# Kernel tuning notes

Measured on AMD Instinct MI355X. Metric: run time of the kernel, lower is better.

Reference implementation:

```python
import jax, jax.numpy as jnp
import numpy as np

FOCAL = 1015.0
IMG = 256


def setup_inputs() -> dict:
    key = jax.random.key(0)
    ks = jax.random.split(key, 9)
    B, NV, NF = 128, 35709, 70789
    coeff = jax.random.normal(ks[0], (B, 257), jnp.float32) * 0.1
    meanshape = jax.random.normal(ks[1], (NV * 3,), jnp.float32)
    idBase = jax.random.normal(ks[2], (NV * 3, 80), jnp.float32) * 0.01
    exBase = jax.random.normal(ks[3], (NV * 3, 64), jnp.float32) * 0.01
    meantex = jax.random.uniform(ks[4], (NV * 3,), jnp.float32) * 255.0
    texBase = jax.random.normal(ks[5], (NV * 3, 80), jnp.float32)
    # 1-based indices, matching the facemodel convention (code subtracts 1)
    tri = jax.random.randint(ks[6], (NF, 3), 1, NV + 1, jnp.int32)
    # point_buf may reference the appended zero face (index NF+1, 1-based)
    point_buf = jax.random.randint(ks[7], (NV, 8), 1, NF + 2, jnp.int32)
    kp_inds = jax.random.randint(ks[8], (68,), 0, NV, jnp.int32)
    return dict(coeff=coeff, meanshape=meanshape, idBase=idBase, exBase=exBase,
                meantex=meantex, texBase=texBase, tri=tri, point_buf=point_buf,
                kp_inds=kp_inds)


def _rotation(angles):
    # rotation = (Rz @ Ry @ Rx)^T, per Compute_rotation_matrix
    sx, sy, sz = jnp.sin(angles[:, 0]), jnp.sin(angles[:, 1]), jnp.sin(angles[:, 2])
    cx, cy, cz = jnp.cos(angles[:, 0]), jnp.cos(angles[:, 1]), jnp.cos(angles[:, 2])
    o, l = jnp.zeros_like(sx), jnp.ones_like(sx)
    Rx = jnp.stack([l, o, o, o, cx, -sx, o, sx, cx], -1).reshape(-1, 3, 3)
    Ry = jnp.stack([cy, o, sy, o, l, o, -sy, o, cy], -1).reshape(-1, 3, 3)
    Rz = jnp.stack([cz, -sz, o, sz, cz, o, o, o, l], -1).reshape(-1, 3, 3)
    return jnp.einsum('bij,bjk,bkl->bli', Rz, Ry, Rx)


def _compute_norm(shape, tri, point_buf):
    fid = tri - 1  # [F,3] 0-based vertex ids
    v1 = shape[:, fid[:, 0]]  # [B,F,3]
    v2 = shape[:, fid[:, 1]]
    v3 = shape[:, fid[:, 2]]
    fn = jnp.cross(v1 - v2, v2 - v3)  # per-face normals [B,F,3]
    fn = jnp.concatenate([fn, jnp.zeros_like(fn[:, :1])], axis=1)  # pad zero face
    vn = fn[:, point_buf - 1].sum(axis=2)  # [B,NV,8,3] -> [B,NV,3]
    return vn / jnp.linalg.norm(vn, axis=2, keepdims=True)


def _illumination(tex, norm, gamma):
    B, N, _ = tex.shape
    gamma = gamma.reshape(B, 3, 9).at[:, :, 0].add(0.8).transpose(0, 2, 1)  # [B,9,3]
    a0 = np.pi
    a1 = 2.0 * np.pi / np.sqrt(3.0)
    a2 = 2.0 * np.pi / np.sqrt(8.0)
    c0 = 1.0 / np.sqrt(4.0 * np.pi)
    c1 = np.sqrt(3.0) / np.sqrt(4.0 * np.pi)
    c2 = 3.0 * np.sqrt(5.0) / np.sqrt(12.0 * np.pi)
    d0 = 0.5 / np.sqrt(3.0)
    nx, ny, nz = norm[..., 0], norm[..., 1], norm[..., 2]
    Y = jnp.stack([
        jnp.full_like(nx, np.float32(a0 * c0)),
        -a1 * c1 * ny,
        a1 * c1 * nz,
        -a1 * c1 * nx,
        a2 * c2 * nx * ny,
        -a2 * c2 * ny * nz,
        a2 * c2 * d0 * (3.0 * nz ** 2 - 1.0),
        -a2 * c2 * nx * nz,
        a2 * c2 * 0.5 * (nx ** 2 - ny ** 2),
    ], axis=-1)  # [B,N,9]
    lighting = jnp.einsum('bnc,bcd->bnd', Y, gamma)  # [B,N,3]
    return tex * lighting


def _project(pts):
    half = IMG // 2
    pts = pts * jnp.array([1.0, 1.0, -1.0], jnp.float32) + jnp.array([0.0, 0.0, 10.0], jnp.float32)
    P = jnp.array([[FOCAL, 0.0, half], [0.0, FOCAL, half], [0.0, 0.0, 1.0]], jnp.float32)
    aug = pts @ P.T
    return aug[..., :2] / aug[..., 2:3]


def reference(coeff, meanshape, idBase, exBase, meantex, texBase, tri, point_buf, kp_inds):
    B = coeff.shape[0]
    idc, exc, texc = coeff[:, :80], coeff[:, 80:144], coeff[:, 144:224]
    angles, gamma, trans = coeff[:, 224:227], coeff[:, 227:254], coeff[:, 254:257]
    # Shape_formation
    shape = (idc @ idBase.T + exc @ exBase.T + meanshape).reshape(B, -1, 3)
    shape = shape - meanshape.reshape(1, -1, 3).mean(axis=1, keepdims=True)
    # Texture_formation
    tex = (texc @ texBase.T + meantex).reshape(B, -1, 3)
    # Normals, rotation, rigid transform
    vnorm = _compute_norm(shape, tri, point_buf)
    rot = _rotation(angles)  # [B,3,3]
    vnorm_r = jnp.einsum('bnc,bcd->bnd', vnorm, rot)
    shape_t = jnp.einsum('bnc,bcd->bnd', shape, rot) + trans[:, None, :]
    # Illumination (vertex colors) and landmark projection
    face_color = _illumination(tex, vnorm_r, gamma)
    lms = _project(shape_t[:, kp_inds])
    lms = jnp.stack([lms[..., 0], IMG - lms[..., 1]], axis=-1)
    return face_color, lms, shape_t
```

## Files before the change

### kernel.cpp

```cpp
#include <hip/hip_runtime.h>

typedef unsigned short u16;
typedef unsigned int u32;
typedef __attribute__((ext_vector_type(8))) short bfrag;
typedef __attribute__((ext_vector_type(4))) float ffrag;
typedef __attribute__((ext_vector_type(4))) float f4;
typedef __attribute__((ext_vector_type(2))) float f2;
typedef __attribute__((ext_vector_type(2))) u32 u32x2;
typedef __attribute__((ext_vector_type(4))) int i4;

#define NVERT 35709
#define NFACE 70789
#define NV3   107127
#define NB    128

#define SHAPE_OFF 0ull
#define TEX4_OFF  54849024ull
#define FXY_OFF   91415040ull
#define FZ_OFF    127659008ull
#define CPACK_OFF 145780992ull
#define MPAD_OFF  145846528ull
#define GG_OFF    145852672ull
#define MEAN_OFF  145866496ull
#define PART_OFF  145866512ull

#define LMS_BASE  13712256ull
#define ST_BASE   13729664ull

__device__ __forceinline__ float b2f(u16 s) {
  union { unsigned u; float f; } v; v.u = ((unsigned)s) << 16; return v.f;
}
__device__ __forceinline__ u16 f2b(float x) {
  union { float f; unsigned u; } v; v.f = x;
  unsigned r = v.u + 0x7FFFu + ((v.u >> 16) & 1u);
  return (u16)(r >> 16);
}
__device__ __forceinline__ u16 h2b(float x) {
  union { _Float16 h; u16 u; } v; v.h = (_Float16)x; return v.u;
}
__device__ __forceinline__ float hb2f(u16 u) {
  union { _Float16 h; u16 u2; } v; v.u2 = u; return (float)v.h;
}
__device__ __forceinline__ f4 ld4u(const float* p) {
  f4 r; __builtin_memcpy(&r, p, 16); return r;
}
__device__ __forceinline__ bfrag cvt8c(const float* p) {
  f4 a = *(const f4*)p;
  f4 b = *(const f4*)(p + 4);
  bfrag r;
  r[0] = (short)f2b(a.x); r[1] = (short)f2b(a.y); r[2] = (short)f2b(a.z); r[3] = (short)f2b(a.w);
  r[4] = (short)f2b(b.x); r[5] = (short)f2b(b.y); r[6] = (short)f2b(b.z); r[7] = (short)f2b(b.w);
  return r;
}

__global__ __launch_bounds__(256) void k_mean(const float* __restrict__ ms, float* __restrict__ part) {
  __shared__ float s[3];
  if (threadIdx.x < 3) s[threadIdx.x] = 0.f;
  __syncthreads();
  float a0 = 0.f, a1 = 0.f, a2 = 0.f;
  for (int v = blockIdx.x * 256 + threadIdx.x; v < NVERT; v += 64 * 256) {
    a0 += ms[v * 3 + 0];
    a1 += ms[v * 3 + 1];
    a2 += ms[v * 3 + 2];
  }
  atomicAdd(&s[0], a0); atomicAdd(&s[1], a1); atomicAdd(&s[2], a2);
  __syncthreads();
  if (threadIdx.x < 3) part[blockIdx.x * 3 + threadIdx.x] = s[threadIdx.x];
}

__global__ __launch_bounds__(128) void k_params(const float* __restrict__ coeff, u16* __restrict__ cpack,
                                                float* __restrict__ mpad, float* __restrict__ G,
                                                const float* __restrict__ part, float* __restrict__ mean) {
  int b = threadIdx.x;
  if (b < 3) {
    float s = 0.f;
    for (int i = 0; i < 64; i++) s += part[i * 3 + b];
    mean[b] = s * (1.0f / (float)NVERT);
  }
  const float* c = coeff + b * 257;
  u16* cp = cpack + b * 256;
  for (int k = 0; k < 80; k++) cp[k] = f2b(c[k]);
  for (int k = 80; k < 96; k++) cp[k] = 0;
  for (int k = 0; k < 64; k++) cp[96 + k] = f2b(c[80 + k]);
  for (int k = 0; k < 80; k++) cp[160 + k] = f2b(c[144 + k]);
  for (int k = 240; k < 256; k++) cp[k] = 0;
  float ax = c[224], ay = c[225], az = c[226];
  float sx = sinf(ax), cx = cosf(ax);
  float sy = sinf(ay), cy = cosf(ay);
  float sz = sinf(az), cz = cosf(az);
  float* mp = mpad + b * 12;
  mp[0] = cz * cy;  mp[1] = cz * sy * sx - sz * cx;  mp[2] = sz * sx + cz * sy * cx;
  mp[3] = sz * cy;  mp[4] = cz * cx + sz * sy * sx;  mp[5] = sz * sy * cx - cz * sx;
  mp[6] = -sy;      mp[7] = cy * sx;                 mp[8] = cy * cx;
  mp[9] = c[254]; mp[10] = c[255]; mp[11] = c[256];
  float* g = G + b * 27;
  for (int cc = 0; cc < 9; cc++)
    for (int d = 0; d < 3; d++)
      g[cc * 3 + d] = c[227 + d * 9 + cc] + (cc == 0 ? 0.8f : 0.0f);
}

#define SBLK 558
__global__ __launch_bounds__(256) void k_gemmS(const float* __restrict__ idB, const float* __restrict__ exB,
                                               const float* __restrict__ ms, const u16* __restrict__ cpack,
                                               const float* __restrict__ meanc, const float* __restrict__ mpad,
                                               float* __restrict__ shp, float* __restrict__ out) {
  __shared__ float SW[4][2][480];
  int jblk = blockIdx.x % SBLK, split = blockIdx.x / SBLK;
  int wave = threadIdx.x >> 6, lane = threadIdx.x & 63;
  int col = lane & 15, quad = lane >> 4;
  int jb = (jblk * 4 + wave) * 48;
  bfrag z8 = {0, 0, 0, 0, 0, 0, 0, 0};
  bfrag bid[3][3], bex[3][2];
  float msj[3], mcv[3];
#pragma unroll
  for (int T = 0; T < 3; T++) {
    int j = jb + T * 16 + col;
    int jc = j < NV3 ? j : NV3 - 1;
    const float* rowI = idB + (size_t)jc * 80;
    const float* rowE = exB + (size_t)jc * 64;
#pragma unroll
    for (int f = 0; f < 3; f++) {
      int k = f * 32 + quad * 8;
      bool ok = (k < 80);
      int ks = ok ? k : 0;
      bfrag vi = cvt8c(rowI + ks);
      bid[T][f] = ok ? vi : z8;
    }
#pragma unroll
    for (int f = 0; f < 2; f++) bex[T][f] = cvt8c(rowE + f * 32 + quad * 8);
    msj[T] = ms[jc];
    mcv[T] = meanc[jc % 3];
  }
  float (*SWl)[480] = SW[wave];
  int s0 = quad >> 1;
  int rb = (quad & 1) << 2;
  int vb = jb / 3;
  int ilim = NV3 - jb; ilim = (ilim > 48 ? 48 : ilim) * 8;
  int vlim = NVERT - vb; vlim = vlim > 16 ? 16 : vlim;

  for (int bt = split * 4; bt < split * 4 + 4; bt++) {
    const u16* cp = cpack + (size_t)(bt * 16 + col) * 256;
#pragma unroll
    for (int T = 0; T < 3; T++) {
      ffrag acc = {0.f, 0.f, 0.f, 0.f};
#pragma unroll
      for (int f = 0; f < 3; f++) {
        bfrag a = *(const bfrag*)(cp + f * 32 + quad * 8);
        acc = __builtin_amdgcn_mfma_f32_16x16x32_bf16(a, bid[T][f], acc, 0, 0, 0);
      }
#pragma unroll
      for (int f = 0; f < 2; f++) {
        bfrag a = *(const bfrag*)(cp + 96 + f * 32 + quad * 8);
        acc = __builtin_amdgcn_mfma_f32_16x16x32_bf16(a, bex[T][f], acc, 0, 0, 0);
      }
#pragma unroll
      for (int rr = 0; rr < 2; rr++) {
        f2 v2;
        v2.x = acc[2 * rr] + msj[T] - mcv[T];
        v2.y = acc[2 * rr + 1] + msj[T] - mcv[T];
        *(f2*)&SWl[s0][(T * 16 + col) * 10 + rb + 2 * rr] = v2;
      }
    }
#pragma unroll
    for (int s = 0; s < 2; s++) {
      size_t sb = (size_t)(bt * 2 + s) * (size_t)(NV3 * 8) + (size_t)jb * 8;
#pragma unroll
      for (int it = 0; it < 3; it++) {
        int i = it * 128 + lane * 2;
        if (i < ilim) {
          f2 vv = *(f2*)&SWl[s][(i >> 3) * 10 + (i & 7)];
          __builtin_nontemporal_store(vv, (f2*)(shp + sb + i));
        }
      }
    }
#pragma unroll
    for (int s = 0; s < 2; s++) {
#pragma unroll
      for (int kk = 0; kk < 2; kk++) {
        int bi = (lane >> 4) + (kk << 2);
        int vloc = lane & 15;
        int b = bt * 16 + s * 8 + bi;
        float x = SWl[s][vloc * 30 + bi];
        float y = SWl[s][vloc * 30 + 10 + bi];
        float z = SWl[s][vloc * 30 + 20 + bi];
        const float* mp = mpad + b * 12;
        f4 m0 = *(const f4*)mp;
        f4 m1 = *(const f4*)(mp + 4);
        f4 m2 = *(const f4*)(mp + 8);
        if (vloc < vlim) {
          float ox = x * m0.x + y * m0.y + z * m0.z + m2.y;
          float oy = x * m0.w + y * m1.x + z * m1.y + m2.z;
          float oz = x * m1.z + y * m1.w + z * m2.x + m2.w;
          size_t o = ST_BASE + (size_t)b * NV3 + (size_t)(vb + vloc) * 3;
          __builtin_nontemporal_store(ox, out + o);
          __builtin_nontemporal_store(oy, out + o + 1);
          __builtin_nontemporal_store(oz, out + o + 2);
        }
      }
    }
  }
}

__global__ __launch_bounds__(256) void k_gemmT(const float* __restrict__ txB, const float* __restrict__ mt,
                                               const u16* __restrict__ cpack, u32* __restrict__ tex4) {
  __shared__ u16 TW[4][2][480];
  int jblk = blockIdx.x % SBLK, split = blockIdx.x / SBLK;
  int wave = threadIdx.x >> 6, lane = threadIdx.x & 63;
  int col = lane & 15, quad = lane >> 4;
  int jb = (jblk * 4 + wave) * 48;
  bfrag z8 = {0, 0, 0, 0, 0, 0, 0, 0};
  bfrag btx[3][3];
  float mtj[3];
#pragma unroll
  for (int T = 0; T < 3; T++) {
    int j = jb + T * 16 + col;
    int jc = j < NV3 ? j : NV3 - 1;
    const float* rowT = txB + (size_t)jc * 80;
#pragma unroll
    for (int f = 0; f < 3; f++) {
      int k = f * 32 + quad * 8;
      bool ok = (k < 80);
      int ks = ok ? k : 0;
      bfrag vt = cvt8c(rowT + ks);
      btx[T][f] = ok ? vt : z8;
    }
    mtj[T] = mt[jc];
  }
  u16 (*TWl)[480] = TW[wave];
  int s0 = quad >> 1;
  int rb = (quad & 1) << 2;
  int vb = jb / 3;
  int vlim = NVERT - vb; vlim = vlim > 16 ? 16 : vlim;

  for (int bt = split * 4; bt < split * 4 + 4; bt++) {
    const u16* cp = cpack + (size_t)(bt * 16 + col) * 256;
#pragma unroll
    for (int T = 0; T < 3; T++) {
      ffrag acc = {0.f, 0.f, 0.f, 0.f};
#pragma unroll
      for (int f = 0; f < 3; f++) {
        bfrag a = *(const bfrag*)(cp + 160 + f * 32 + quad * 8);
        acc = __builtin_amdgcn_mfma_f32_16x16x32_bf16(a, btx[T][f], acc, 0, 0, 0);
      }
#pragma unroll
      for (int rr = 0; rr < 2; rr++) {
        TWl[s0][(T * 16 + col) * 10 + rb + 2 * rr]     = f2b(acc[2 * rr] + mtj[T]);
        TWl[s0][(T * 16 + col) * 10 + rb + 2 * rr + 1] = f2b(acc[2 * rr + 1] + mtj[T]);
      }
    }
#pragma unroll
    for (int s = 0; s < 2; s++) {
#pragma unroll
      for (int kk = 0; kk < 2; kk++) {
        int bi = (lane >> 4) + (kk << 2);
        int vloc = lane & 15;
        if (vloc < vlim) {
          u16 x = TWl[s][vloc * 30 + bi];
          u16 y = TWl[s][vloc * 30 + 10 + bi];
          u16 z = TWl[s][vloc * 30 + 20 + bi];
          u32x2 val;
          val.x = (u32)x | ((u32)y << 16);
          val.y = (u32)z;
          size_t idx = (((size_t)(bt * 2 + s) * NVERT + (vb + vloc)) * 8 + bi) * 2;
          __builtin_nontemporal_store(val, (u32x2*)(tex4 + idx));
        }
      }
    }
  }
}

#define FN_CH2 2213
__global__ __launch_bounds__(256) void k_fn(const float* __restrict__ shpT, const int* __restrict__ tri,
                                            u32* __restrict__ fxy, u16* __restrict__ fz, int lo) {
  int g = blockIdx.x;
  int xcd = g & 7, chunk = g >> 3;
  int bt8 = lo + xcd;
  int t = threadIdx.x;
  int bi = t & 7, foff = t >> 3;
  int f = chunk * 32 + foff;
  if (f >= NFACE) return;
  int i0 = tri[f * 3 + 0] - 1;
  int i1 = tri[f * 3 + 1] - 1;
  int i2 = tri[f * 3 + 2] - 1;
  const float* sl = shpT + (size_t)bt8 * (size_t)(NV3 * 8);
  int a0 = i0 * 24 + bi, a1 = i1 * 24 + bi, a2 = i2 * 24 + bi;
  float x1 = sl[a0], y1 = sl[a0 + 8], z1 = sl[a0 + 16];
  float x2 = sl[a1], y2 = sl[a1 + 8], z2 = sl[a1 + 16];
  float x3 = sl[a2], y3 = sl[a2 + 8], z3 = sl[a2 + 16];
  float e1x = x1 - x2, e1y = y1 - y2, e1z = z1 - z2;
  float e2x = x2 - x3, e2y = y2 - y3, e2z = z2 - z3;
  u16 hx = h2b(e1y * e2z - e1z * e2y);
  u16 hy = h2b(e1z * e2x - e1x * e2z);
  u16 hz = h2b(e1x * e2y - e1y * e2x);
  size_t o = (size_t)bt8 * (size_t)(NFACE * 8) + (size_t)f * 8 + bi;
  fxy[o] = (u32)hx | ((u32)hy << 16);
  fz[o] = hz;
}

#define FI_CH2 1116
__global__ __launch_bounds__(256) void k_final(const u32* __restrict__ tex4, const u32* __restrict__ fxy,
                                               const u16* __restrict__ fz, const int* __restrict__ pbuf,
                                               const float* __restrict__ mpad, const float* __restrict__ G,
                                               float* __restrict__ out, int lo) {
  __shared__ float scol[8][100];
  int g = blockIdx.x;
  int xcd = g & 7, chunk = g >> 3;
  int bt8 = lo + xcd;
  int t = threadIdx.x;
  int bi = t & 7, voff = t >> 3;
  int v0 = chunk * 32;
  int v = v0 + voff;
  int vc = v < NVERT ? v : NVERT - 1;
  bool valid = v < NVERT;
  int b = bt8 * 8 + bi;
  i4 p0 = *(const i4*)(pbuf + (size_t)vc * 8);
  i4 p1 = *(const i4*)(pbuf + (size_t)vc * 8 + 4);
  int idx[8] = {p0.x, p0.y, p0.z, p0.w, p1.x, p1.y, p1.z, p1.w};
  const u32* fx = fxy + (size_t)bt8 * (size_t)(NFACE * 8);
  const u16* fzb = fz + (size_t)bt8 * (size_t)(NFACE * 8);
  float vx = 0.f, vy = 0.f, vz = 0.f;
#pragma unroll
  for (int i = 0; i < 8; i++) {
    int id = idx[i] - 1;
    if (id < NFACE) {
      u32 q = fx[(size_t)id * 8 + bi];
      u16 qz = fzb[(size_t)id * 8 + bi];
      vx += hb2f((u16)q); vy += hb2f((u16)(q >> 16)); vz += hb2f(qz);
    }
  }
  float n2 = vx * vx + vy * vy + vz * vz;
  float inv = rsqrtf(fmaxf(n2, 1e-30f));
  vx *= inv; vy *= inv; vz *= inv;
  const float* mp = mpad + b * 12;
  f4 m0 = *(const f4*)mp;
  f4 m1 = *(const f4*)(mp + 4);
  float m8 = mp[8];
  float nx = vx * m0.x + vy * m0.y + vz * m0.z;
  float ny = vx * m0.w + vy * m1.x + vz * m1.y;
  float nz = vx * m1.z + vy * m1.w + vz * m8;
  const float kc1 = 1.7724539f;
  const float kc2 = 2.4270324f;
  const float kd0 = 0.28867513f;
  float Y[9];
  Y[0] = 0.8862269f;
  Y[1] = -kc1 * ny;
  Y[2] = kc1 * nz;
  Y[3] = -kc1 * nx;
  Y[4] = kc2 * nx * ny;
  Y[5] = -kc2 * ny * nz;
  Y[6] = kc2 * kd0 * (3.f * nz * nz - 1.f);
  Y[7] = -kc2 * nx * nz;
  Y[8] = kc2 * 0.5f * (nx * nx - ny * ny);
  const float* gg = G + b * 27;
  float gv[28];
#pragma unroll
  for (int q = 0; q < 7; q++) {
    f4 g4 = ld4u(gg + q * 4);
    gv[q * 4] = g4.x; gv[q * 4 + 1] = g4.y; gv[q * 4 + 2] = g4.z; gv[q * 4 + 3] = g4.w;
  }
  if (valid) {
    u32x2 tv = __builtin_nontemporal_load(
        (const u32x2*)(tex4 + ((size_t)bt8 * NVERT + vc) * 16 + bi * 2));
    float tc[3] = { b2f((u16)tv.x), b2f((u16)(tv.x >> 16)), b2f((u16)tv.y) };
#pragma unroll
    for (int d = 0; d < 3; d++) {
      float L = 0.f;
#pragma unroll
      for (int cc = 0; cc < 9; cc++) L += Y[cc] * gv[cc * 3 + d];
      scol[bi][voff * 3 + d] = tc[d] * L;
    }
  }
  __syncthreads();
  int nvv = NVERT - v0;
  int lim = (nvv < 32 ? nvv : 32) * 3;
  size_t base = (size_t)(bt8 * 8) * NV3 + (size_t)v0 * 3;
#pragma unroll
  for (int it = 0; it < 3; it++) {
    int l = it * 256 + t;
    int b2 = l / 96, e = l - b2 * 96;
    if (e < lim) {
      size_t o = base + (size_t)b2 * NV3 + e;
      __builtin_nontemporal_store(scol[b2][e], out + o);
    }
  }
}

__global__ __launch_bounds__(128) void k_lms(const float* __restrict__ shpT, const int* __restrict__ kp,
                                             const float* __restrict__ mpad, float* __restrict__ out) {
  int t = threadIdx.x;
  int b = blockIdx.x;
  if (t >= 68) return;
  int v = kp[t];
  const float* sl = shpT + (size_t)(b >> 3) * (size_t)(NV3 * 8) + (size_t)v * 24 + (b & 7);
  float sx = sl[0], sy = sl[8], sz = sl[16];
  const float* mp = mpad + b * 12;
  f4 m0 = *(const f4*)mp;
  f4 m1 = *(const f4*)(mp + 4);
  f4 m2 = *(const f4*)(mp + 8);
  float ox = sx * m0.x + sy * m0.y + sz * m0.z + m2.y;
  float oy = sx * m0.w + sy * m1.x + sz * m1.y + m2.z;
  float oz = sx * m1.z + sy * m1.w + sz * m2.x + m2.w;
  float w = 10.f - oz;
  float invw = 1.0f / w;
  float lx = 1015.f * ox * invw + 128.f;
  float ly = 1015.f * oy * invw + 128.f;
  size_t o = LMS_BASE + ((size_t)b * 68 + t) * 2;
  out[o + 0] = lx;
  out[o + 1] = 256.f - ly;
}

extern "C" void kernel_launch(void* const* d_in, const int* in_sizes, int n_in,
                              void* d_out, int out_size, void* d_ws, size_t ws_size,
                              hipStream_t stream) {
  const float* coeff     = (const float*)d_in[0];
  const float* meanshape = (const float*)d_in[1];
  const float* idB       = (const float*)d_in[2];
  const float* exB       = (const float*)d_in[3];
  const float* meantex   = (const float*)d_in[4];
  const float* txB       = (const float*)d_in[5];
  const int* tri         = (const int*)d_in[6];
  const int* pbuf        = (const int*)d_in[7];
  const int* kp          = (const int*)d_in[8];
  float* out = (float*)d_out;
  char* ws = (char*)d_ws;
  float* shpT = (float*)(ws + SHAPE_OFF);
  u32* tex4   = (u32*)(ws + TEX4_OFF);
  u32* fxy    = (u32*)(ws + FXY_OFF);
  u16* fzp    = (u16*)(ws + FZ_OFF);
  u16* cpack  = (u16*)(ws + CPACK_OFF);
  float* mpad = (float*)(ws + MPAD_OFF);
  float* G    = (float*)(ws + GG_OFF);
  float* mean = (float*)(ws + MEAN_OFF);
  float* part = (float*)(ws + PART_OFF);

  k_mean<<<64, 256, 0, stream>>>(meanshape, part);
  k_params<<<1, 128, 0, stream>>>(coeff, cpack, mpad, G, part, mean);
  k_gemmS<<<2 * SBLK, 256, 0, stream>>>(idB, exB, meanshape, cpack, mean, mpad, shpT, out);
  k_gemmT<<<2 * SBLK, 256, 0, stream>>>(txB, meantex, cpack, tex4);
  for (int lo = 0; lo < 16; lo += 8) {
    k_fn<<<8 * FN_CH2, 256, 0, stream>>>(shpT, tri, fxy, fzp, lo);
    k_final<<<8 * FI_CH2, 256, 0, stream>>>(tex4, fxy, fzp, pbuf, mpad, G, out, lo);
  }
  k_lms<<<128, 128, 0, stream>>>(shpT, kp, mpad, out);
}
```

Before: 423.4 us.

## Reload basis fragments per batch tile to cut registers and raise occupancy

Both GEMM kernels no longer keep the bf16-converted basis fragments in registers across the batch-tile loop. They reload and convert them from global memory on each of the four iterations, with a compiler barrier and unroll 1 to stop the loads being hoisted. Launch bounds now request 8 blocks per CU to force lower register use. This trades four times the basis reads and conversions, mostly served from cache, for higher occupancy and better latency hiding.

Result: slower. 514.6 us (+21.5%).

```diff
diff --git a/kernel.cpp b/kernel.cpp
--- a/kernel.cpp
+++ b/kernel.cpp
@@ -100,36 +100,24 @@
 }
 
 #define SBLK 558
-__global__ __launch_bounds__(256) void k_gemmS(const float* __restrict__ idB, const float* __restrict__ exB,
-                                               const float* __restrict__ ms, const u16* __restrict__ cpack,
-                                               const float* __restrict__ meanc, const float* __restrict__ mpad,
-                                               float* __restrict__ shp, float* __restrict__ out) {
+__global__ __launch_bounds__(256, 8) void k_gemmS(const float* __restrict__ idB, const float* __restrict__ exB,
+                                                  const float* __restrict__ ms, const u16* __restrict__ cpack,
+                                                  const float* __restrict__ meanc, const float* __restrict__ mpad,
+                                                  float* __restrict__ shp, float* __restrict__ out) {
   __shared__ float SW[4][2][480];
   int jblk = blockIdx.x % SBLK, split = blockIdx.x / SBLK;
   int wave = threadIdx.x >> 6, lane = threadIdx.x & 63;
   int col = lane & 15, quad = lane >> 4;
   int jb = (jblk * 4 + wave) * 48;
   bfrag z8 = {0, 0, 0, 0, 0, 0, 0, 0};
-  bfrag bid[3][3], bex[3][2];
-  float msj[3], mcv[3];
+  int jcs[3];
+  float msub[3];
 #pragma unroll
   for (int T = 0; T < 3; T++) {
     int j = jb + T * 16 + col;
     int jc = j < NV3 ? j : NV3 - 1;
-    const float* rowI = idB + (size_t)jc * 80;
-    const float* rowE = exB + (size_t)jc * 64;
-#pragma unroll
-    for (int f = 0; f < 3; f++) {
-      int k = f * 32 + quad * 8;
-      bool ok = (k < 80);
-      int ks = ok ? k : 0;
-      bfrag vi = cvt8c(rowI + ks);
-      bid[T][f] = ok ? vi : z8;
-    }
-#pragma unroll
-    for (int f = 0; f < 2; f++) bex[T][f] = cvt8c(rowE + f * 32 + quad * 8);
-    msj[T] = ms[jc];
-    mcv[T] = meanc[jc % 3];
+    jcs[T] = jc;
+    msub[T] = ms[jc] - meanc[jc % 3];
   }
   float (*SWl)[480] = SW[wave];
   int s0 = quad >> 1;
@@ -138,26 +126,37 @@
   int ilim = NV3 - jb; ilim = (ilim > 48 ? 48 : ilim) * 8;
   int vlim = NVERT - vb; vlim = vlim > 16 ? 16 : vlim;
 
+#pragma unroll 1
   for (int bt = split * 4; bt < split * 4 + 4; bt++) {
+    asm volatile("" ::: "memory");
     const u16* cp = cpack + (size_t)(bt * 16 + col) * 256;
 #pragma unroll
     for (int T = 0; T < 3; T++) {
+      int jc = jcs[T];
+      const float* rowI = idB + (size_t)jc * 80;
+      const float* rowE = exB + (size_t)jc * 64;
       ffrag acc = {0.f, 0.f, 0.f, 0.f};
 #pragma unroll
       for (int f = 0; f < 3; f++) {
+        int k = f * 32 + quad * 8;
+        bool ok = (k < 80);
+        int ks = ok ? k : 0;
+        bfrag bb = cvt8c(rowI + ks);
+        bb = ok ? bb : z8;
         bfrag a = *(const bfrag*)(cp + f * 32 + quad * 8);
-        acc = __builtin_amdgcn_mfma_f32_16x16x32_bf16(a, bid[T][f], acc, 0, 0, 0);
+        acc = __builtin_amdgcn_mfma_f32_16x16x32_bf16(a, bb, acc, 0, 0, 0);
       }
 #pragma unroll
       for (int f = 0; f < 2; f++) {
+        bfrag bb = cvt8c(rowE + f * 32 + quad * 8);
         bfrag a = *(const bfrag*)(cp + 96 + f * 32 + quad * 8);
-        acc = __builtin_amdgcn_mfma_f32_16x16x32_bf16(a, bex[T][f], acc, 0, 0, 0);
+        acc = __builtin_amdgcn_mfma_f32_16x16x32_bf16(a, bb, acc, 0, 0, 0);
       }
 #pragma unroll
       for (int rr = 0; rr < 2; rr++) {
         f2 v2;
-        v2.x = acc[2 * rr] + msj[T] - mcv[T];
-        v2.y = acc[2 * rr + 1] + msj[T] - mcv[T];
+        v2.x = acc[2 * rr] + msub[T];
+        v2.y = acc[2 * rr + 1] + msub[T];
         *(f2*)&SWl[s0][(T * 16 + col) * 10 + rb + 2 * rr] = v2;
       }
     }
@@ -201,29 +200,21 @@
   }
 }
 
-__global__ __launch_bounds__(256) void k_gemmT(const float* __restrict__ txB, const float* __restrict__ mt,
-                                               const u16* __restrict__ cpack, u32* __restrict__ tex4) {
+__global__ __launch_bounds__(256, 8) void k_gemmT(const float* __restrict__ txB, const float* __restrict__ mt,
+                                                  const u16* __restrict__ cpack, u32* __restrict__ tex4) {
   __shared__ u16 TW[4][2][480];
   int jblk = blockIdx.x % SBLK, split = blockIdx.x / SBLK;
   int wave = threadIdx.x >> 6, lane = threadIdx.x & 63;
   int col = lane & 15, quad = lane >> 4;
   int jb = (jblk * 4 + wave) * 48;
   bfrag z8 = {0, 0, 0, 0, 0, 0, 0, 0};
-  bfrag btx[3][3];
+  int jcs[3];
   float mtj[3];
 #pragma unroll
   for (int T = 0; T < 3; T++) {
     int j = jb + T * 16 + col;
     int jc = j < NV3 ? j : NV3 - 1;
-    const float* rowT = txB + (size_t)jc * 80;
-#pragma unroll
-    for (int f = 0; f < 3; f++) {
-      int k = f * 32 + quad * 8;
-      bool ok = (k < 80);
-      int ks = ok ? k : 0;
-      bfrag vt = cvt8c(rowT + ks);
-      btx[T][f] = ok ? vt : z8;
-    }
+    jcs[T] = jc;
     mtj[T] = mt[jc];
   }
   u16 (*TWl)[480] = TW[wave];
@@ -232,15 +223,24 @@
   int vb = jb / 3;
   int vlim = NVERT - vb; vlim = vlim > 16 ? 16 : vlim;
 
+#pragma unroll 1
   for (int bt = split * 4; bt < split * 4 + 4; bt++) {
+    asm volatile("" ::: "memory");
     const u16* cp = cpack + (size_t)(bt * 16 + col) * 256;
 #pragma unroll
     for (int T = 0; T < 3; T++) {
+      int jc = jcs[T];
+      const float* rowT = txB + (size_t)jc * 80;
       ffrag acc = {0.f, 0.f, 0.f, 0.f};
 #pragma unroll
       for (int f = 0; f < 3; f++) {
+        int k = f * 32 + quad * 8;
+        bool ok = (k < 80);
+        int ks = ok ? k : 0;
+        bfrag bb = cvt8c(rowT + ks);
+        bb = ok ? bb : z8;
         bfrag a = *(const bfrag*)(cp + 160 + f * 32 + quad * 8);
-        acc = __builtin_amdgcn_mfma_f32_16x16x32_bf16(a, btx[T][f], acc, 0, 0, 0);
+        acc = __builtin_amdgcn_mfma_f32_16x16x32_bf16(a, bb, acc, 0, 0, 0);
       }
 #pragma unroll
       for (int rr = 0; rr < 2; rr++) {
```

## Pack face normals as fp16 quads and process two batch items per thread

Applied to the files above, without the earlier changes.

Face normals are now stored as one 8-byte fp16 record (x,y,z,pad) per face and batch item, replacing the split u32 xy and u16 z arrays, so each gather in the normal accumulation becomes a single 16-byte load covering two batch items. k_fn and k_final each handle two batch elements per thread with vectorized f2 loads, which halves the thread count per face or vertex and doubles the tile size. The texture GEMM now writes the same batch-interleaved layout as the shape buffer, which makes its stores coalesced. The cost is more registers per thread in k_final and a padded fq buffer about a third larger, which may reduce occupancy.

Result: faster. 408.9 us (-3.4%).

```diff
diff --git a/kernel.cpp b/kernel.cpp
--- a/kernel.cpp
+++ b/kernel.cpp
@@ -6,8 +6,9 @@
 typedef __attribute__((ext_vector_type(4))) float ffrag;
 typedef __attribute__((ext_vector_type(4))) float f4;
 typedef __attribute__((ext_vector_type(2))) float f2;
-typedef __attribute__((ext_vector_type(2))) u32 u32x2;
 typedef __attribute__((ext_vector_type(4))) int i4;
+typedef __attribute__((ext_vector_type(4))) _Float16 h4;
+typedef __attribute__((ext_vector_type(8))) _Float16 h8;
 
 #define NVERT 35709
 #define NFACE 70789
@@ -15,14 +16,13 @@
 #define NB    128
 
 #define SHAPE_OFF 0ull
-#define TEX4_OFF  54849024ull
-#define FXY_OFF   91415040ull
-#define FZ_OFF    127659008ull
-#define CPACK_OFF 145780992ull
-#define MPAD_OFF  145846528ull
-#define GG_OFF    145852672ull
-#define MEAN_OFF  145866496ull
-#define PART_OFF  145866512ull
+#define TEX_OFF   54849024ull
+#define FQ_OFF    82273536ull
+#define CPACK_OFF 154761472ull
+#define MPAD_OFF  154827008ull
+#define GG_OFF    154833152ull
+#define MEAN_OFF  154846976ull
+#define PART_OFF  154846992ull
 
 #define LMS_BASE  13712256ull
 #define ST_BASE   13729664ull
@@ -34,12 +34,6 @@
   union { float f; unsigned u; } v; v.f = x;
   unsigned r = v.u + 0x7FFFu + ((v.u >> 16) & 1u);
   return (u16)(r >> 16);
-}
-__device__ __forceinline__ u16 h2b(float x) {
-  union { _Float16 h; u16 u; } v; v.h = (_Float16)x; return v.u;
-}
-__device__ __forceinline__ float hb2f(u16 u) {
-  union { _Float16 h; u16 u2; } v; v.u2 = u; return (float)v.h;
 }
 __device__ __forceinline__ f4 ld4u(const float* p) {
   f4 r; __builtin_memcpy(&r, p, 16); return r;
@@ -111,7 +105,7 @@
   int jb = (jblk * 4 + wave) * 48;
   bfrag z8 = {0, 0, 0, 0, 0, 0, 0, 0};
   bfrag bid[3][3], bex[3][2];
-  float msj[3], mcv[3];
+  float msub[3];
 #pragma unroll
   for (int T = 0; T < 3; T++) {
     int j = jb + T * 16 + col;
@@ -128,8 +122,7 @@
     }
 #pragma unroll
     for (int f = 0; f < 2; f++) bex[T][f] = cvt8c(rowE + f * 32 + quad * 8);
-    msj[T] = ms[jc];
-    mcv[T] = meanc[jc % 3];
+    msub[T] = ms[jc] - meanc[jc % 3];
   }
   float (*SWl)[480] = SW[wave];
   int s0 = quad >> 1;
@@ -156,8 +149,8 @@
 #pragma unroll
       for (int rr = 0; rr < 2; rr++) {
         f2 v2;
-        v2.x = acc[2 * rr] + msj[T] - mcv[T];
-        v2.y = acc[2 * rr + 1] + msj[T] - mcv[T];
+        v2.x = acc[2 * rr] + msub[T];
+        v2.y = acc[2 * rr + 1] + msub[T];
         *(f2*)&SWl[s0][(T * 16 + col) * 10 + rb + 2 * rr] = v2;
       }
     }
@@ -202,7 +195,7 @@
 }
 
 __global__ __launch_bounds__(256) void k_gemmT(const float* __restrict__ txB, const float* __restrict__ mt,
-                                               const u16* __restrict__ cpack, u32* __restrict__ tex4) {
+                                               const u16* __restrict__ cpack, u16* __restrict__ texo) {
   __shared__ u16 TW[4][2][480];
   int jblk = blockIdx.x % SBLK, split = blockIdx.x / SBLK;
   int wave = threadIdx.x >> 6, lane = threadIdx.x & 63;
@@ -229,8 +222,7 @@
   u16 (*TWl)[480] = TW[wave];
   int s0 = quad >> 1;
   int rb = (quad & 1) << 2;
-  int vb = jb / 3;
-  int vlim = NVERT - vb; vlim = vlim > 16 ? 16 : vlim;
+  int ilim = NV3 - jb; ilim = (ilim > 48 ? 48 : ilim) * 8;
 
   for (int bt = split * 4; bt < split * 4 + 4; bt++) {
     const u16* cp = cpack + (size_t)(bt * 16 + col) * 256;
@@ -250,134 +242,138 @@
     }
 #pragma unroll
     for (int s = 0; s < 2; s++) {
-#pragma unroll
-      for (int kk = 0; kk < 2; kk++) {
-        int bi = (lane >> 4) + (kk << 2);
-        int vloc = lane & 15;
-        if (vloc < vlim) {
-          u16 x = TWl[s][vloc * 30 + bi];
-          u16 y = TWl[s][vloc * 30 + 10 + bi];
-          u16 z = TWl[s][vloc * 30 + 20 + bi];
-          u32x2 val;
-          val.x = (u32)x | ((u32)y << 16);
-          val.y = (u32)z;
-          size_t idx = (((size_t)(bt * 2 + s) * NVERT + (vb + vloc)) * 8 + bi) * 2;
-          __builtin_nontemporal_store(val, (u32x2*)(tex4 + idx));
+      size_t sb = (size_t)(bt * 2 + s) * (size_t)(NV3 * 8) + (size_t)jb * 8;
+#pragma unroll
+      for (int it = 0; it < 3; it++) {
+        int i = it * 128 + lane * 2;
+        if (i < ilim) {
+          int li = (i >> 3) * 10 + (i & 7);
+          u32 val = (u32)TWl[s][li] | ((u32)TWl[s][li + 1] << 16);
+          __builtin_nontemporal_store(val, (u32*)(texo + sb + i));
         }
       }
     }
   }
 }
 
-#define FN_CH2 2213
+#define FN_CH3 1107
 __global__ __launch_bounds__(256) void k_fn(const float* __restrict__ shpT, const int* __restrict__ tri,
-                                            u32* __restrict__ fxy, u16* __restrict__ fz, int lo) {
+                                            h4* __restrict__ fq, int lo) {
   int g = blockIdx.x;
   int xcd = g & 7, chunk = g >> 3;
   int bt8 = lo + xcd;
   int t = threadIdx.x;
-  int bi = t & 7, foff = t >> 3;
-  int f = chunk * 32 + foff;
+  int bp = t & 3, foff = t >> 2;
+  int f = chunk * 64 + foff;
   if (f >= NFACE) return;
   int i0 = tri[f * 3 + 0] - 1;
   int i1 = tri[f * 3 + 1] - 1;
   int i2 = tri[f * 3 + 2] - 1;
-  const float* sl = shpT + (size_t)bt8 * (size_t)(NV3 * 8);
-  int a0 = i0 * 24 + bi, a1 = i1 * 24 + bi, a2 = i2 * 24 + bi;
-  float x1 = sl[a0], y1 = sl[a0 + 8], z1 = sl[a0 + 16];
-  float x2 = sl[a1], y2 = sl[a1 + 8], z2 = sl[a1 + 16];
-  float x3 = sl[a2], y3 = sl[a2 + 8], z3 = sl[a2 + 16];
-  float e1x = x1 - x2, e1y = y1 - y2, e1z = z1 - z2;
-  float e2x = x2 - x3, e2y = y2 - y3, e2z = z2 - z3;
-  u16 hx = h2b(e1y * e2z - e1z * e2y);
-  u16 hy = h2b(e1z * e2x - e1x * e2z);
-  u16 hz = h2b(e1x * e2y - e1y * e2x);
-  size_t o = (size_t)bt8 * (size_t)(NFACE * 8) + (size_t)f * 8 + bi;
-  fxy[o] = (u32)hx | ((u32)hy << 16);
-  fz[o] = hz;
-}
-
-#define FI_CH2 1116
-__global__ __launch_bounds__(256) void k_final(const u32* __restrict__ tex4, const u32* __restrict__ fxy,
-                                               const u16* __restrict__ fz, const int* __restrict__ pbuf,
-                                               const float* __restrict__ mpad, const float* __restrict__ G,
-                                               float* __restrict__ out, int lo) {
-  __shared__ float scol[8][100];
+  const float* sl = shpT + (size_t)bt8 * (size_t)(NV3 * 8) + 2 * bp;
+  int a0 = i0 * 24, a1 = i1 * 24, a2 = i2 * 24;
+  f2 x1 = *(const f2*)(sl + a0), y1 = *(const f2*)(sl + a0 + 8), z1 = *(const f2*)(sl + a0 + 16);
+  f2 x2 = *(const f2*)(sl + a1), y2 = *(const f2*)(sl + a1 + 8), z2 = *(const f2*)(sl + a1 + 16);
+  f2 x3 = *(const f2*)(sl + a2), y3 = *(const f2*)(sl + a2 + 8), z3 = *(const f2*)(sl + a2 + 16);
+  f2 e1x = x1 - x2, e1y = y1 - y2, e1z = z1 - z2;
+  f2 e2x = x2 - x3, e2y = y2 - y3, e2z = z2 - z3;
+  f2 cx = e1y * e2z - e1z * e2y;
+  f2 cy = e1z * e2x - e1x * e2z;
+  f2 cz = e1x * e2y - e1y * e2x;
+  h8 st;
+  st[0] = (_Float16)cx.x; st[1] = (_Float16)cy.x; st[2] = (_Float16)cz.x; st[3] = (_Float16)0.f;
+  st[4] = (_Float16)cx.y; st[5] = (_Float16)cy.y; st[6] = (_Float16)cz.y; st[7] = (_Float16)0.f;
+  *(h8*)(fq + (size_t)bt8 * (size_t)(NFACE * 8) + (size_t)f * 8 + 2 * bp) = st;
+}
+
+#define FI_CH3 558
+__global__ __launch_bounds__(256) void k_final(const u16* __restrict__ texT, const h4* __restrict__ fq,
+                                               const int* __restrict__ pbuf, const float* __restrict__ mpad,
+                                               const float* __restrict__ G, float* __restrict__ out, int lo) {
+  __shared__ float scol[8][200];
   int g = blockIdx.x;
   int xcd = g & 7, chunk = g >> 3;
   int bt8 = lo + xcd;
   int t = threadIdx.x;
-  int bi = t & 7, voff = t >> 3;
-  int v0 = chunk * 32;
+  int bp = t & 3, voff = t >> 2;
+  int v0 = chunk * 64;
   int v = v0 + voff;
   int vc = v < NVERT ? v : NVERT - 1;
   bool valid = v < NVERT;
-  int b = bt8 * 8 + bi;
   i4 p0 = *(const i4*)(pbuf + (size_t)vc * 8);
   i4 p1 = *(const i4*)(pbuf + (size_t)vc * 8 + 4);
   int idx[8] = {p0.x, p0.y, p0.z, p0.w, p1.x, p1.y, p1.z, p1.w};
-  const u32* fx = fxy + (size_t)bt8 * (size_t)(NFACE * 8);
-  const u16* fzb = fz + (size_t)bt8 * (size_t)(NFACE * 8);
-  float vx = 0.f, vy = 0.f, vz = 0.f;
+  const h4* fb = fq + (size_t)bt8 * (size_t)(NFACE * 8) + 2 * bp;
+  float vx0 = 0.f, vy0 = 0.f, vz0 = 0.f, vx1 = 0.f, vy1 = 0.f, vz1 = 0.f;
 #pragma unroll
   for (int i = 0; i < 8; i++) {
     int id = idx[i] - 1;
     if (id < NFACE) {
-      u32 q = fx[(size_t)id * 8 + bi];
-      u16 qz = fzb[(size_t)id * 8 + bi];
-      vx += hb2f((u16)q); vy += hb2f((u16)(q >> 16)); vz += hb2f(qz);
-    }
-  }
-  float n2 = vx * vx + vy * vy + vz * vz;
-  float inv = rsqrtf(fmaxf(n2, 1e-30f));
-  vx *= inv; vy *= inv; vz *= inv;
-  const float* mp = mpad + b * 12;
-  f4 m0 = *(const f4*)mp;
-  f4 m1 = *(const f4*)(mp + 4);
-  float m8 = mp[8];
-  float nx = vx * m0.x + vy * m0.y + vz * m0.z;
-  float ny = vx * m0.w + vy * m1.x + vz * m1.y;
-  float nz = vx * m1.z + vy * m1.w + vz * m8;
+      h8 q = *(const h8*)(fb + (size_t)id * 8);
+      vx0 += (float)q[0]; vy0 += (float)q[1]; vz0 += (float)q[2];
+      vx1 += (float)q[4]; vy1 += (float)q[5]; vz1 += (float)q[6];
+    }
+  }
+  const u16* tp = texT + (size_t)bt8 * (size_t)(NV3 * 8) + (size_t)vc * 24 + 2 * bp;
+  u32 t0 = *(const u32*)(tp);
+  u32 t1 = *(const u32*)(tp + 8);
+  u32 t2 = *(const u32*)(tp + 16);
   const float kc1 = 1.7724539f;
   const float kc2 = 2.4270324f;
   const float kd0 = 0.28867513f;
-  float Y[9];
-  Y[0] = 0.8862269f;
-  Y[1] = -kc1 * ny;
-  Y[2] = kc1 * nz;
-  Y[3] = -kc1 * nx;
-  Y[4] = kc2 * nx * ny;
-  Y[5] = -kc2 * ny * nz;
-  Y[6] = kc2 * kd0 * (3.f * nz * nz - 1.f);
-  Y[7] = -kc2 * nx * nz;
-  Y[8] = kc2 * 0.5f * (nx * nx - ny * ny);
-  const float* gg = G + b * 27;
-  float gv[28];
-#pragma unroll
-  for (int q = 0; q < 7; q++) {
-    f4 g4 = ld4u(gg + q * 4);
-    gv[q * 4] = g4.x; gv[q * 4 + 1] = g4.y; gv[q * 4 + 2] = g4.z; gv[q * 4 + 3] = g4.w;
-  }
-  if (valid) {
-    u32x2 tv = __builtin_nontemporal_load(
-        (const u32x2*)(tex4 + ((size_t)bt8 * NVERT + vc) * 16 + bi * 2));
-    float tc[3] = { b2f((u16)tv.x), b2f((u16)(tv.x >> 16)), b2f((u16)tv.y) };
-#pragma unroll
-    for (int d = 0; d < 3; d++) {
-      float L = 0.f;
-#pragma unroll
-      for (int cc = 0; cc < 9; cc++) L += Y[cc] * gv[cc * 3 + d];
-      scol[bi][voff * 3 + d] = tc[d] * L;
+#pragma unroll
+  for (int pp = 0; pp < 2; pp++) {
+    int bi = 2 * bp + pp;
+    int b = bt8 * 8 + bi;
+    float vx = pp ? vx1 : vx0, vy = pp ? vy1 : vy0, vz = pp ? vz1 : vz0;
+    float n2 = vx * vx + vy * vy + vz * vz;
+    float inv = rsqrtf(fmaxf(n2, 1e-30f));
+    vx *= inv; vy *= inv; vz *= inv;
+    const float* mp = mpad + b * 12;
+    f4 m0 = *(const f4*)mp;
+    f4 m1 = *(const f4*)(mp + 4);
+    float m8 = mp[8];
+    float nx = vx * m0.x + vy * m0.y + vz * m0.z;
+    float ny = vx * m0.w + vy * m1.x + vz * m1.y;
+    float nz = vx * m1.z + vy * m1.w + vz * m8;
+    float Y[9];
+    Y[0] = 0.8862269f;
+    Y[1] = -kc1 * ny;
+    Y[2] = kc1 * nz;
+    Y[3] = -kc1 * nx;
+    Y[4] = kc2 * nx * ny;
+    Y[5] = -kc2 * ny * nz;
+    Y[6] = kc2 * kd0 * (3.f * nz * nz - 1.f);
+    Y[7] = -kc2 * nx * nz;
+    Y[8] = kc2 * 0.5f * (nx * nx - ny * ny);
+    const float* gg = G + b * 27;
+    float gv[28];
+#pragma unroll
+    for (int q = 0; q < 7; q++) {
+      f4 g4 = ld4u(gg + q * 4);
+      gv[q * 4] = g4.x; gv[q * 4 + 1] = g4.y; gv[q * 4 + 2] = g4.z; gv[q * 4 + 3] = g4.w;
+    }
+    float tc[3];
+    tc[0] = b2f((u16)(pp ? (t0 >> 16) : t0));
+    tc[1] = b2f((u16)(pp ? (t1 >> 16) : t1));
+    tc[2] = b2f((u16)(pp ? (t2 >> 16) : t2));
+    if (valid) {
+#pragma unroll
+      for (int d = 0; d < 3; d++) {
+        float L = 0.f;
+#pragma unroll
+        for (int cc = 0; cc < 9; cc++) L += Y[cc] * gv[cc * 3 + d];
+        scol[bi][voff * 3 + d] = tc[d] * L;
+      }
     }
   }
   __syncthreads();
   int nvv = NVERT - v0;
-  int lim = (nvv < 32 ? nvv : 32) * 3;
+  int lim = (nvv < 64 ? nvv : 64) * 3;
   size_t base = (size_t)(bt8 * 8) * NV3 + (size_t)v0 * 3;
 #pragma unroll
-  for (int it = 0; it < 3; it++) {
+  for (int it = 0; it < 6; it++) {
     int l = it * 256 + t;
-    int b2 = l / 96, e = l - b2 * 96;
+    int b2 = l / 192, e = l - b2 * 192;
     if (e < lim) {
       size_t o = base + (size_t)b2 * NV3 + e;
       __builtin_nontemporal_store(scol[b2][e], out + o);
@@ -424,9 +420,8 @@
   float* out = (float*)d_out;
   char* ws = (char*)d_ws;
   float* shpT = (float*)(ws + SHAPE_OFF);
-  u32* tex4   = (u32*)(ws + TEX4_OFF);
-  u32* fxy    = (u32*)(ws + FXY_OFF);
-  u16* fzp    = (u16*)(ws + FZ_OFF);
+  u16* texT   = (u16*)(ws + TEX_OFF);
+  h4* fq      = (h4*)(ws + FQ_OFF);
   u16* cpack  = (u16*)(ws + CPACK_OFF);
   float* mpad = (float*)(ws + MPAD_OFF);
   float* G    = (float*)(ws + GG_OFF);
@@ -436,10 +431,10 @@
   k_mean<<<64, 256, 0, stream>>>(meanshape, part);
   k_params<<<1, 128, 0, stream>>>(coeff, cpack, mpad, G, part, mean);
   k_gemmS<<<2 * SBLK, 256, 0, stream>>>(idB, exB, meanshape, cpack, mean, mpad, shpT, out);
-  k_gemmT<<<2 * SBLK, 256, 0, stream>>>(txB, meantex, cpack, tex4);
+  k_gemmT<<<2 * SBLK, 256, 0, stream>>>(txB, meantex, cpack, texT);
   for (int lo = 0; lo < 16; lo += 8) {
-    k_fn<<<8 * FN_CH2, 256, 0, stream>>>(shpT, tri, fxy, fzp, lo);
-    k_final<<<8 * FI_CH2, 256, 0, stream>>>(tex4, fxy, fzp, pbuf, mpad, G, out, lo);
+    k_fn<<<8 * FN_CH3, 256, 0, stream>>>(shpT, tri, fq, lo);
+    k_final<<<8 * FI_CH3, 256, 0, stream>>>(texT, fq, pbuf, mpad, G, out, lo);
   }
   k_lms<<<128, 128, 0, stream>>>(shpT, kp, mpad, out);
 }
```
